# Kernel tuning notes

Measured on AMD Instinct MI355X. Metric: run time of the kernel, lower is better.

Reference implementation:

```python
import jax, jax.numpy as jnp
import numpy as np

B, S, D, H = 4, 2048, 1024, 16
DK = D // H  # 64


def setup_inputs() -> dict:
    key = jax.random.key(0)
    ks = jax.random.split(key, 12)
    sc = 0.02
    return {
        "q": jax.random.normal(ks[0], (B, S, D), jnp.float32),
        "k": jax.random.normal(ks[1], (B, S, D), jnp.float32),
        "v": jax.random.normal(ks[2], (B, S, D), jnp.float32),
        "mask": jax.random.randint(ks[3], (B, S, S), 0, 2).astype(bool),
        "Wq": jax.random.normal(ks[4], (H, D, DK), jnp.float32) * sc,
        "bq": jax.random.normal(ks[5], (H, DK), jnp.float32) * sc,
        "Wk": jax.random.normal(ks[6], (H, D, DK), jnp.float32) * sc,
        "bk": jax.random.normal(ks[7], (H, DK), jnp.float32) * sc,
        "Wv": jax.random.normal(ks[8], (H, D, DK), jnp.float32) * sc,
        "bv": jax.random.normal(ks[9], (H, DK), jnp.float32) * sc,
        "Wo": jax.random.normal(ks[10], (D, D), jnp.float32) * sc,
        "bo": jax.random.normal(ks[11], (D,), jnp.float32) * sc,
    }


def reference(q, k, v, mask, Wq, bq, Wk, bk, Wv, bv, Wo, bo):
    # per-head projections, batched over heads: [b,s,d] x [h,d,k] -> [b,h,s,k]
    qh = jnp.einsum('bsd,hdk->bhsk', q, Wq) + bq[None, :, None, :]
    kh = jnp.einsum('bsd,hdk->bhsk', k, Wk) + bk[None, :, None, :]
    vh = jnp.einsum('bsd,hdk->bhsk', v, Wv) + bv[None, :, None, :]
    dk = qh.shape[-1]
    scores = jnp.einsum('bhsk,bhtk->bhst', qh, kh) / (dk ** 0.5)
    # original uses masked_fill(mask == False, -1e-06) -- NOT -inf; keep faithful
    scores = jnp.where(mask[:, None, :, :], scores, jnp.float32(-1e-06))
    attn = jax.nn.softmax(scores, axis=-1)
    out = jnp.einsum('bhst,bhtk->bhsk', attn, vh)
    b, h, s, _ = out.shape
    out = out.transpose(0, 2, 1, 3).reshape(b, s, h * dk)  # concat heads
    return out @ Wo + bo
```

## Files before the change

### kernel.cpp

```cpp
#include <hip/hip_runtime.h>
#include <stdint.h>

#define Bn 4
#define Sn 2048
#define Dn 1024
#define Hn 16
#define DKn 64

typedef __bf16 bf16x8 __attribute__((ext_vector_type(8)));
typedef float f32x4 __attribute__((ext_vector_type(4)));
typedef unsigned short u16;
typedef unsigned long long u64;

union ABFrag { bf16x8 v; uint4 u; };
union V8 { u16 us[8]; uint4 u; };

__device__ __forceinline__ u16 f2bf(float f) {
  union { float f; uint32_t u; } a; a.f = f;
  return (u16)((a.u + 0x7fffu + ((a.u >> 16) & 1u)) >> 16);
}

__device__ __forceinline__ void gload16(const void* g, void* l) {
  __builtin_amdgcn_global_load_lds((const __attribute__((address_space(1))) unsigned int*)g,
                                   (__attribute__((address_space(3))) unsigned int*)l, 16, 0, 0);
}

__device__ __forceinline__ f32x4 zero4() { f32x4 z; z[0]=0.f; z[1]=0.f; z[2]=0.f; z[3]=0.f; return z; }


__global__ void conv_bf16(const float* __restrict__ src, u16* __restrict__ dst, int n4) {
  int i = blockIdx.x * 256 + threadIdx.x;
  if (i < n4) {
    float4 v = ((const float4*)src)[i];
    V8 o;
    o.us[0] = f2bf(v.x); o.us[1] = f2bf(v.y); o.us[2] = f2bf(v.z); o.us[3] = f2bf(v.w);
    ((uint2*)dst)[i] = make_uint2(o.u.x, o.u.y);
  }
}

__device__ __forceinline__ void tile_tr_body(const float* __restrict__ s, int ss,
                                             u16* __restrict__ d, int ds) {
  __shared__ float t[64 * 65];
  int tid = threadIdx.x;
  int r = tid >> 2, c0 = (tid & 3) * 16;
  #pragma unroll
  for (int j = 0; j < 4; ++j) {
    float4 v = *(const float4*)(s + r * ss + c0 + j * 4);
    t[(c0 + j * 4 + 0) * 65 + r] = v.x;
    t[(c0 + j * 4 + 1) * 65 + r] = v.y;
    t[(c0 + j * 4 + 2) * 65 + r] = v.z;
    t[(c0 + j * 4 + 3) * 65 + r] = v.w;
  }
  __syncthreads();
  V8 o0, o1;
  #pragma unroll
  for (int j = 0; j < 8; ++j) o0.us[j] = f2bf(t[r * 65 + c0 + j]);
  #pragma unroll
  for (int j = 0; j < 8; ++j) o1.us[j] = f2bf(t[r * 65 + c0 + 8 + j]);
  *(uint4*)(d + r * ds + c0) = o0.u;
  *(uint4*)(d + r * ds + c0 + 8) = o1.u;
}

__global__ void prep_wqkv_t(const float* __restrict__ Wq, const float* __restrict__ Wk,
                            const float* __restrict__ Wv, u16* __restrict__ out) {
  int bid = blockIdx.x;
  int w = bid >> 8, h = (bid >> 4) & 15, db = bid & 15;
  const float* src = (w == 0) ? Wq : (w == 1) ? Wk : Wv;
  tile_tr_body(src + (h * 1024 + db * 64) * 64, 64,
               out + (size_t)(w * 1024 + h * 64) * 1024 + db * 64, 1024);
}

__global__ void prep_wo_t(const float* __restrict__ Wo, u16* __restrict__ out) {
  int bid = blockIdx.x;
  int rb = bid >> 4, cb = bid & 15;
  tile_tr_body(Wo + (size_t)rb * 64 * 1024 + cb * 64, 1024,
               out + (size_t)cb * 64 * 1024 + rb * 64, 1024);
}

__global__ void mask_detect(const uint32_t* __restrict__ mw, int* __restrict__ flag) {
  int t = threadIdx.x;
  uint32_t acc = 0;
  for (int j = 0; j < 4; ++j) acc |= (mw[t * 4 + j] > 1u) ? 1u : 0u;
  unsigned long long bal = __ballot(acc != 0);
  __shared__ int s[4];
  if ((t & 63) == 0) s[t >> 6] = (bal != 0ull) ? 1 : 0;
  __syncthreads();
  if (t == 0) *flag = s[0] | s[1] | s[2] | s[3];
}

__global__ void mask_pack(const void* __restrict__ mraw, const int* __restrict__ flag,
                          u64* __restrict__ mb, int nwords) {
  int i = blockIdx.x * 256 + threadIdx.x;
  if (i >= nwords) return;
  u64 w = 0;
  if (*flag) {
    const uchar4* p = (const uchar4*)mraw + (size_t)i * 16;
    #pragma unroll
    for (int j = 0; j < 16; ++j) {
      uchar4 v = p[j];
      w |= ((u64)(v.x != 0)) << (j * 4 + 0);
      w |= ((u64)(v.y != 0)) << (j * 4 + 1);
      w |= ((u64)(v.z != 0)) << (j * 4 + 2);
      w |= ((u64)(v.w != 0)) << (j * 4 + 3);
    }
  } else {
    const uint4* p = (const uint4*)mraw + (size_t)i * 16;
    #pragma unroll
    for (int j = 0; j < 16; ++j) {
      uint4 v = p[j];
      w |= ((u64)(v.x != 0)) << (j * 4 + 0);
      w |= ((u64)(v.y != 0)) << (j * 4 + 1);
      w |= ((u64)(v.z != 0)) << (j * 4 + 2);
      w |= ((u64)(v.w != 0)) << (j * 4 + 3);
    }
  }
  mb[i] = w;
}

__global__ void transpose_v(const u16* __restrict__ vh, u16* __restrict__ vt) {
  __shared__ char lds[64 * 128];
  int tid = threadIdx.x;
  int bh = blockIdx.y, s0 = blockIdx.x * 64;
  const char* src = (const char*)(vh + ((size_t)bh * Sn + s0) * DKn);
  #pragma unroll
  for (int si = 0; si < 2; ++si) {
    int c = si * 256 + tid, r = c >> 3, cb = c & 7;
    uint4 v = *(const uint4*)(src + r * 128 + cb * 16);
    *(uint4*)(lds + r * 128 + ((cb ^ (r & 7)) << 4)) = v;
  }
  __syncthreads();
  #pragma unroll
  for (int si = 0; si < 2; ++si) {
    int c = si * 256 + tid, dkr = c >> 3, sb = c & 7;
    V8 t;
    #pragma unroll
    for (int j = 0; j < 8; ++j) {
      int s = sb * 8 + j;
      t.us[j] = *(const u16*)(lds + s * 128 + ((dkr * 2) ^ ((s & 7) << 4)));
    }
    *(uint4*)(vt + ((size_t)bh * DKn + dkr) * Sn + s0 + sb * 8) = t.u;
  }
}

template<int MODE>
__launch_bounds__(256)
__global__ void gemm_kernel(const u16* __restrict__ Aq, const u16* __restrict__ Ak,
                            const u16* __restrict__ Av, const u16* __restrict__ Bm,
                            const float* __restrict__ bq, const float* __restrict__ bk,
                            const float* __restrict__ bv,
                            u16* __restrict__ Oq, u16* __restrict__ Ok, u16* __restrict__ Ov,
                            float* __restrict__ Of) {
  __shared__ char lds[32768];
  char* Al = lds;
  char* Bl = lds + 16384;
  const int tid = threadIdx.x, w = tid >> 6, lane = tid & 63;
  const int n0 = blockIdx.x * 128, m0 = blockIdx.y * 128;
  int which = 0;
  const u16* A = Aq;
  if (MODE == 0) { which = n0 >> 10; A = (which == 0) ? Aq : (which == 1) ? Ak : Av; }

  f32x4 acc[2][8];
  #pragma unroll
  for (int i = 0; i < 2; ++i)
    #pragma unroll
    for (int j = 0; j < 8; ++j) acc[i][j] = zero4();

  for (int kt = 0; kt < 16; ++kt) {
    __syncthreads();
    #pragma unroll
    for (int si = 0; si < 4; ++si) {
      int c = si * 256 + tid, r = c >> 3, cb = c & 7;
      gload16((const char*)A + (((size_t)(m0 + r)) << 11) + (size_t)(kt * 128) + ((cb ^ (r & 7)) << 4),
              Al + si * 4096 + w * 1024);
    }
    #pragma unroll
    for (int si = 0; si < 4; ++si) {
      int c = si * 256 + tid, r = c >> 3, cb = c & 7;
      gload16((const char*)Bm + (((size_t)(n0 + r)) << 11) + (size_t)(kt * 128) + ((cb ^ (r & 7)) << 4),
              Bl + si * 4096 + w * 1024);
    }
    __syncthreads();
    #pragma unroll
    for (int kk = 0; kk < 2; ++kk) {
      ABFrag a0, a1;
      {
        int row = w * 32 + (lane & 15);
        int ch = (lane >> 4) + kk * 4;
        a0.u = *(const uint4*)(Al + row * 128 + ((ch ^ (row & 7)) << 4));
        row += 16;
        a1.u = *(const uint4*)(Al + row * 128 + ((ch ^ (row & 7)) << 4));
      }
      #pragma unroll
      for (int nn = 0; nn < 8; ++nn) {
        int row = nn * 16 + (lane & 15);
        int ch = (lane >> 4) + kk * 4;
        ABFrag bb; bb.u = *(const uint4*)(Bl + row * 128 + ((ch ^ (row & 7)) << 4));
        acc[0][nn] = __builtin_amdgcn_mfma_f32_16x16x32_bf16(a0.v, bb.v, acc[0][nn], 0, 0, 0);
        acc[1][nn] = __builtin_amdgcn_mfma_f32_16x16x32_bf16(a1.v, bb.v, acc[1][nn], 0, 0, 0);
      }
    }
  }

  if (MODE == 0) {
    const float esc = (which == 0) ? 0.18033688011112042f : 1.0f;
    const float* bias = (which == 0) ? bq : (which == 1) ? bk : bv;
    u16* O = (which == 0) ? Oq : (which == 1) ? Ok : Ov;
    #pragma unroll
    for (int nn = 0; nn < 8; ++nn) {
      int ng = (n0 & 1023) + nn * 16 + (lane & 15);
      int h = ng >> 6, dk = ng & 63;
      float bsv = bias[ng];
      #pragma unroll
      for (int mm = 0; mm < 2; ++mm) {
        #pragma unroll
        for (int r = 0; r < 4; ++r) {
          int mg = m0 + w * 32 + mm * 16 + (lane >> 4) * 4 + r;
          int b = mg >> 11, s = mg & 2047;
          O[(((size_t)(b * Hn + h)) * Sn + s) * DKn + dk] = f2bf((acc[mm][nn][r] + bsv) * esc);
        }
      }
    }
  } else {
    #pragma unroll
    for (int nn = 0; nn < 8; ++nn) {
      int ng = n0 + nn * 16 + (lane & 15);
      float bsv = bq[ng];
      #pragma unroll
      for (int mm = 0; mm < 2; ++mm) {
        #pragma unroll
        for (int r = 0; r < 4; ++r) {
          int mg = m0 + w * 32 + mm * 16 + (lane >> 4) * 4 + r;
          Of[(size_t)mg * 1024 + ng] = acc[mm][nn][r] + bsv;
        }
      }
    }
  }
}

__launch_bounds__(256, 4)
__global__ void flash_attn(const u16* __restrict__ qh, const u16* __restrict__ kh,
                           const u16* __restrict__ vt, const u64* __restrict__ mb,
                           u16* __restrict__ o) {
  __shared__ char lds[24576];
  char* Klds = lds;
  char* Vlds = lds + 8192;
  const int tid = threadIdx.x, w = tid >> 6, lane = tid & 63;
  const int l15 = lane & 15, g = lane >> 4;
  char* Plds = lds + 16384 + w * 2048;

  int bid = blockIdx.x;
  int wg = (bid & 7) * 256 + (bid >> 3);
  const int bh = wg >> 5, b = bh >> 4, h = bh & 15;
  const int qr = (wg & 31) * 64 + w * 16;

  ABFrag aq0, aq1;
  {
    const char* qrow = (const char*)(qh + ((size_t)bh * Sn + qr + l15) * DKn);
    aq0.u = *(const uint4*)(qrow + g * 16);
    aq1.u = *(const uint4*)(qrow + 64 + g * 16);
  }

  const char* kbase = (const char*)(kh + (size_t)bh * Sn * DKn);
  const char* vbase = (const char*)(vt + (size_t)bh * DKn * Sn);
  const int rowg = qr + g * 4;
  const char* mp = (const char*)mb + ((size_t)b * Sn + rowg) * 256;

  f32x4 oacc[4];
  float psum[4];
  #pragma unroll
  for (int nn = 0; nn < 4; ++nn) oacc[nn] = zero4();
  #pragma unroll
  for (int r = 0; r < 4; ++r) psum[r] = 0.f;

  const int sr = (256 + tid) >> 3, scb = (256 + tid) & 7;
  const int r0 = tid >> 3, cb0 = tid & 7;
  const int pw_base = (g * 4) * 128;
  const int pr_base = l15 * 128;
  const int pr_sw   = (l15 & 7) << 4;

  for (int kt = 0; kt < Sn / 64; ++kt) {
    u64 mw0 = *(const u64*)(mp + kt * 8);
    u64 mw1 = *(const u64*)(mp + kt * 8 + 256);
    u64 mw2 = *(const u64*)(mp + kt * 8 + 512);
    u64 mw3 = *(const u64*)(mp + kt * 8 + 768);

    __syncthreads();
    gload16(kbase + (size_t)(kt * 64 + r0) * 128 + ((cb0 ^ (r0 & 7)) << 4),
            Klds + w * 1024);
    gload16(kbase + (size_t)(kt * 64 + sr) * 128 + ((scb ^ (sr & 7)) << 4),
            Klds + 4096 + w * 1024);
    gload16(vbase + (size_t)r0 * (Sn * 2) + (size_t)(kt * 128) + ((cb0 ^ (r0 & 7)) << 4),
            Vlds + w * 1024);
    gload16(vbase + (size_t)sr * (Sn * 2) + (size_t)(kt * 128) + ((scb ^ (sr & 7)) << 4),
            Vlds + 4096 + w * 1024);
    __syncthreads();

    f32x4 sacc[4];
    #pragma unroll
    for (int nn = 0; nn < 4; ++nn) sacc[nn] = zero4();
    #pragma unroll
    for (int kk = 0; kk < 2; ++kk) {
      ABFrag aq = (kk == 0) ? aq0 : aq1;
      #pragma unroll
      for (int nn = 0; nn < 4; ++nn) {
        int row = nn * 16 + l15;
        int ch = g + kk * 4;
        ABFrag kf; kf.u = *(const uint4*)(Klds + row * 128 + ((ch ^ (row & 7)) << 4));
        sacc[nn] = __builtin_amdgcn_mfma_f32_16x16x32_bf16(aq.v, kf.v, sacc[nn], 0, 0, 0);
      }
    }

    #pragma unroll
    for (int r = 0; r < 4; ++r) {
      u64 mwr = (r == 0) ? mw0 : (r == 1) ? mw1 : (r == 2) ? mw2 : mw3;
      int prow = pw_base + r * 128;
      int psw = (((g * 4 + r) & 7) << 4);
      #pragma unroll
      for (int nn = 0; nn < 4; ++nn) {
        float pe = __builtin_amdgcn_exp2f(sacc[nn][r]);
        unsigned m16 = (unsigned)(mwr >> (nn * 16)) & 0xffffu;
        float pv = ((m16 >> l15) & 1u) ? pe : 1.0f;
        psum[r] += pv;
        *(__bf16*)(Plds + prow + (((nn * 32) + l15 * 2) ^ psw)) = (__bf16)pv;
      }
    }

    #pragma unroll
    for (int kk = 0; kk < 2; ++kk) {
      ABFrag pa;
      pa.u = *(const uint4*)(Plds + pr_base + ((kk * 64 + g * 16) ^ pr_sw));
      #pragma unroll
      for (int nn = 0; nn < 4; ++nn) {
        int row = nn * 16 + l15;
        int ch = g + kk * 4;
        ABFrag vb; vb.u = *(const uint4*)(Vlds + row * 128 + ((ch ^ (row & 7)) << 4));
        oacc[nn] = __builtin_amdgcn_mfma_f32_16x16x32_bf16(pa.v, vb.v, oacc[nn], 0, 0, 0);
      }
    }
  }

  #pragma unroll
  for (int r = 0; r < 4; ++r) {
    float s = psum[r];
    s += __shfl_xor(s, 1, 16);
    s += __shfl_xor(s, 2, 16);
    s += __shfl_xor(s, 4, 16);
    s += __shfl_xor(s, 8, 16);
    float inv = 1.f / s;
    int sg = qr + g * 4 + r;
    #pragma unroll
    for (int nn = 0; nn < 4; ++nn) {
      int col = h * 64 + nn * 16 + l15;
      o[((size_t)(b * Sn) + sg) * Dn + col] = f2bf(oacc[nn][r] * inv);
    }
  }
}


extern "C" void kernel_launch(void* const* d_in, const int* in_sizes, int n_in,
                              void* d_out, int out_size, void* d_ws, size_t ws_size,
                              hipStream_t stream) {
  (void)in_sizes; (void)n_in; (void)out_size; (void)ws_size;
  const float* q  = (const float*)d_in[0];
  const float* k  = (const float*)d_in[1];
  const float* v  = (const float*)d_in[2];
  const void*  mask = d_in[3];
  const float* Wq = (const float*)d_in[4];
  const float* bq = (const float*)d_in[5];
  const float* Wk = (const float*)d_in[6];
  const float* bk = (const float*)d_in[7];
  const float* Wv = (const float*)d_in[8];
  const float* bv = (const float*)d_in[9];
  const float* Wo = (const float*)d_in[10];
  const float* bo = (const float*)d_in[11];
  float* out = (float*)d_out;

  char* ws = (char*)d_ws;
  const size_t SZ = (size_t)8192 * 1024 * 2;
  u16* qbf   = (u16*)(ws);
  u16* kbf   = (u16*)(ws + SZ);
  u16* vbf   = (u16*)(ws + 2 * SZ);
  u16* Wcatt = (u16*)(ws + 3 * SZ);
  u16* Wot   = (u16*)(ws + 3 * SZ + 6291456);
  u16* qhp   = (u16*)(ws + 3 * SZ + 8388608);
  u16* khp   = (u16*)((char*)qhp + SZ);
  u16* vhp   = (u16*)((char*)khp + SZ);
  int* flag  = (int*)((char*)vhp + SZ);

  conv_bf16<<<8192, 256, 0, stream>>>(q, qbf, 2097152);
  conv_bf16<<<8192, 256, 0, stream>>>(k, kbf, 2097152);
  conv_bf16<<<8192, 256, 0, stream>>>(v, vbf, 2097152);
  prep_wqkv_t<<<768, 256, 0, stream>>>(Wq, Wk, Wv, Wcatt);
  prep_wo_t<<<256, 256, 0, stream>>>(Wo, Wot);

  gemm_kernel<0><<<dim3(24, 64), 256, 0, stream>>>(qbf, kbf, vbf, Wcatt, bq, bk, bv,
                                                   qhp, khp, vhp, nullptr);

  mask_detect<<<1, 256, 0, stream>>>((const uint32_t*)mask, flag);
  u64* mbw = (u64*)vbf;
  mask_pack<<<1024, 256, 0, stream>>>(mask, flag, mbw, 262144);

  u16* vtb = kbf;
  transpose_v<<<dim3(32, 64), 256, 0, stream>>>(vhp, vtb);

  u16* oc = qbf;
  flash_attn<<<2048, 256, 0, stream>>>(qhp, khp, vtb, mbw, oc);

  gemm_kernel<1><<<dim3(8, 64), 256, 0, stream>>>(oc, nullptr, nullptr, Wot, bo,
                                                  nullptr, nullptr, nullptr,
                                                  nullptr, nullptr, out);
}
```

Before: 453.5 us.

## Double-buffer K/V loads in flash attention, fuse prep kernels, write V transposed

Flash attention now prefetches the next K/V tile into a second LDS buffer while computing on the current one, with explicit waitcnt and barriers replacing the two syncthreads per tile. The three bf16 conversion launches are merged into one, as are the two weight-transpose launches. The V projection epilogue writes V directly in transposed layout, so the separate transpose_v kernel is dropped. The transposed V writes are strided 2-byte stores, which may coalesce poorly in the GEMM epilogue, and the larger LDS footprint may lower attention occupancy.

Measured after the change: 464.4 us. +2.4%, slower.

```diff
diff --git a/kernel.cpp b/kernel.cpp
--- a/kernel.cpp
+++ b/kernel.cpp
@@ -28,14 +28,17 @@
 __device__ __forceinline__ f32x4 zero4() { f32x4 z; z[0]=0.f; z[1]=0.f; z[2]=0.f; z[3]=0.f; return z; }
 
 
-__global__ void conv_bf16(const float* __restrict__ src, u16* __restrict__ dst, int n4) {
+__global__ void conv_bf16_all(const float* __restrict__ q, const float* __restrict__ k,
+                              const float* __restrict__ v, u16* __restrict__ dq,
+                              u16* __restrict__ dk, u16* __restrict__ dv) {
   int i = blockIdx.x * 256 + threadIdx.x;
-  if (i < n4) {
-    float4 v = ((const float4*)src)[i];
-    V8 o;
-    o.us[0] = f2bf(v.x); o.us[1] = f2bf(v.y); o.us[2] = f2bf(v.z); o.us[3] = f2bf(v.w);
-    ((uint2*)dst)[i] = make_uint2(o.u.x, o.u.y);
-  }
+  int seg = i >> 21, j = i & 2097151;
+  const float* s = (seg == 0) ? q : (seg == 1) ? k : v;
+  u16* d = (seg == 0) ? dq : (seg == 1) ? dk : dv;
+  float4 vv = ((const float4*)s)[j];
+  V8 o;
+  o.us[0] = f2bf(vv.x); o.us[1] = f2bf(vv.y); o.us[2] = f2bf(vv.z); o.us[3] = f2bf(vv.w);
+  ((uint2*)d)[j] = make_uint2(o.u.x, o.u.y);
 }
 
 __device__ __forceinline__ void tile_tr_body(const float* __restrict__ s, int ss,
@@ -61,20 +64,21 @@
   *(uint4*)(d + r * ds + c0 + 8) = o1.u;
 }
 
-__global__ void prep_wqkv_t(const float* __restrict__ Wq, const float* __restrict__ Wk,
-                            const float* __restrict__ Wv, u16* __restrict__ out) {
+__global__ void prep_w_all(const float* __restrict__ Wq, const float* __restrict__ Wk,
+                           const float* __restrict__ Wv, const float* __restrict__ Wo,
+                           u16* __restrict__ wcatt, u16* __restrict__ wot) {
   int bid = blockIdx.x;
-  int w = bid >> 8, h = (bid >> 4) & 15, db = bid & 15;
-  const float* src = (w == 0) ? Wq : (w == 1) ? Wk : Wv;
-  tile_tr_body(src + (h * 1024 + db * 64) * 64, 64,
-               out + (size_t)(w * 1024 + h * 64) * 1024 + db * 64, 1024);
-}
-
-__global__ void prep_wo_t(const float* __restrict__ Wo, u16* __restrict__ out) {
-  int bid = blockIdx.x;
-  int rb = bid >> 4, cb = bid & 15;
-  tile_tr_body(Wo + (size_t)rb * 64 * 1024 + cb * 64, 1024,
-               out + (size_t)cb * 64 * 1024 + rb * 64, 1024);
+  if (bid < 768) {
+    int w = bid >> 8, h = (bid >> 4) & 15, db = bid & 15;
+    const float* src = (w == 0) ? Wq : (w == 1) ? Wk : Wv;
+    tile_tr_body(src + (h * 1024 + db * 64) * 64, 64,
+                 wcatt + (size_t)(w * 1024 + h * 64) * 1024 + db * 64, 1024);
+  } else {
+    int b2 = bid - 768;
+    int rb = b2 >> 4, cb = b2 & 15;
+    tile_tr_body(Wo + (size_t)rb * 64 * 1024 + cb * 64, 1024,
+                 wot + (size_t)cb * 64 * 1024 + rb * 64, 1024);
+  }
 }
 
 __global__ void mask_detect(const uint32_t* __restrict__ mw, int* __restrict__ flag) {
@@ -115,31 +119,6 @@
     }
   }
   mb[i] = w;
-}
-
-__global__ void transpose_v(const u16* __restrict__ vh, u16* __restrict__ vt) {
-  __shared__ char lds[64 * 128];
-  int tid = threadIdx.x;
-  int bh = blockIdx.y, s0 = blockIdx.x * 64;
-  const char* src = (const char*)(vh + ((size_t)bh * Sn + s0) * DKn);
-  #pragma unroll
-  for (int si = 0; si < 2; ++si) {
-    int c = si * 256 + tid, r = c >> 3, cb = c & 7;
-    uint4 v = *(const uint4*)(src + r * 128 + cb * 16);
-    *(uint4*)(lds + r * 128 + ((cb ^ (r & 7)) << 4)) = v;
-  }
-  __syncthreads();
-  #pragma unroll
-  for (int si = 0; si < 2; ++si) {
-    int c = si * 256 + tid, dkr = c >> 3, sb = c & 7;
-    V8 t;
-    #pragma unroll
-    for (int j = 0; j < 8; ++j) {
-      int s = sb * 8 + j;
-      t.us[j] = *(const u16*)(lds + s * 128 + ((dkr * 2) ^ ((s & 7) << 4)));
-    }
-    *(uint4*)(vt + ((size_t)bh * DKn + dkr) * Sn + s0 + sb * 8) = t.u;
-  }
 }
 
 template<int MODE>
@@ -204,7 +183,6 @@
   if (MODE == 0) {
     const float esc = (which == 0) ? 0.18033688011112042f : 1.0f;
     const float* bias = (which == 0) ? bq : (which == 1) ? bk : bv;
-    u16* O = (which == 0) ? Oq : (which == 1) ? Ok : Ov;
     #pragma unroll
     for (int nn = 0; nn < 8; ++nn) {
       int ng = (n0 & 1023) + nn * 16 + (lane & 15);
@@ -216,7 +194,13 @@
         for (int r = 0; r < 4; ++r) {
           int mg = m0 + w * 32 + mm * 16 + (lane >> 4) * 4 + r;
           int b = mg >> 11, s = mg & 2047;
-          O[(((size_t)(b * Hn + h)) * Sn + s) * DKn + dk] = f2bf((acc[mm][nn][r] + bsv) * esc);
+          float val = (acc[mm][nn][r] + bsv) * esc;
+          if (which == 2) {
+            Ov[(((size_t)((b * Hn + h) * DKn + dk)) << 11) + s] = f2bf(val);
+          } else {
+            u16* O = (which == 0) ? Oq : Ok;
+            O[(((size_t)(b * Hn + h)) * Sn + s) * DKn + dk] = f2bf(val);
+          }
         }
       }
     }
@@ -241,12 +225,10 @@
 __global__ void flash_attn(const u16* __restrict__ qh, const u16* __restrict__ kh,
                            const u16* __restrict__ vt, const u64* __restrict__ mb,
                            u16* __restrict__ o) {
-  __shared__ char lds[24576];
-  char* Klds = lds;
-  char* Vlds = lds + 8192;
+  __shared__ char lds[40960];
   const int tid = threadIdx.x, w = tid >> 6, lane = tid & 63;
   const int l15 = lane & 15, g = lane >> 4;
-  char* Plds = lds + 16384 + w * 2048;
+  char* Plds = lds + 32768 + w * 2048;
 
   int bid = blockIdx.x;
   int wg = (bid & 7) * 256 + (bid >> 3);
@@ -272,28 +254,47 @@
   #pragma unroll
   for (int r = 0; r < 4; ++r) psum[r] = 0.f;
 
+  const int r0 = tid >> 3, cb0 = tid & 7;
   const int sr = (256 + tid) >> 3, scb = (256 + tid) & 7;
-  const int r0 = tid >> 3, cb0 = tid & 7;
   const int pw_base = (g * 4) * 128;
   const int pr_base = l15 * 128;
   const int pr_sw   = (l15 & 7) << 4;
 
+  gload16(kbase + (size_t)r0 * 128 + ((cb0 ^ (r0 & 7)) << 4), lds + w * 1024);
+  gload16(kbase + (size_t)sr * 128 + ((scb ^ (sr & 7)) << 4), lds + 4096 + w * 1024);
+  gload16(vbase + (size_t)r0 * (Sn * 2) + ((cb0 ^ (r0 & 7)) << 4), lds + 8192 + w * 1024);
+  gload16(vbase + (size_t)sr * (Sn * 2) + ((scb ^ (sr & 7)) << 4), lds + 12288 + w * 1024);
+
   for (int kt = 0; kt < Sn / 64; ++kt) {
+    char* bufK = lds + (kt & 1) * 16384;
+    char* bufV = bufK + 8192;
+    char* nK = lds + ((kt & 1) ^ 1) * 16384;
+    char* nV = nK + 8192;
+
     u64 mw0 = *(const u64*)(mp + kt * 8);
     u64 mw1 = *(const u64*)(mp + kt * 8 + 256);
     u64 mw2 = *(const u64*)(mp + kt * 8 + 512);
     u64 mw3 = *(const u64*)(mp + kt * 8 + 768);
 
-    __syncthreads();
-    gload16(kbase + (size_t)(kt * 64 + r0) * 128 + ((cb0 ^ (r0 & 7)) << 4),
-            Klds + w * 1024);
-    gload16(kbase + (size_t)(kt * 64 + sr) * 128 + ((scb ^ (sr & 7)) << 4),
-            Klds + 4096 + w * 1024);
-    gload16(vbase + (size_t)r0 * (Sn * 2) + (size_t)(kt * 128) + ((cb0 ^ (r0 & 7)) << 4),
-            Vlds + w * 1024);
-    gload16(vbase + (size_t)sr * (Sn * 2) + (size_t)(kt * 128) + ((scb ^ (sr & 7)) << 4),
-            Vlds + 4096 + w * 1024);
-    __syncthreads();
+    asm volatile("s_waitcnt lgkmcnt(0)" ::: "memory");
+    __builtin_amdgcn_sched_barrier(0);
+    __builtin_amdgcn_s_barrier();
+    __builtin_amdgcn_sched_barrier(0);
+
+    if (kt < Sn / 64 - 1) {
+      gload16(kbase + (size_t)((kt + 1) * 64 + r0) * 128 + ((cb0 ^ (r0 & 7)) << 4), nK + w * 1024);
+      gload16(kbase + (size_t)((kt + 1) * 64 + sr) * 128 + ((scb ^ (sr & 7)) << 4), nK + 4096 + w * 1024);
+      gload16(vbase + (size_t)r0 * (Sn * 2) + (size_t)((kt + 1) * 128) + ((cb0 ^ (r0 & 7)) << 4), nV + w * 1024);
+      gload16(vbase + (size_t)sr * (Sn * 2) + (size_t)((kt + 1) * 128) + ((scb ^ (sr & 7)) << 4), nV + 4096 + w * 1024);
+      __builtin_amdgcn_sched_barrier(0);
+      asm volatile("s_waitcnt vmcnt(8)" ::: "memory");
+    } else {
+      __builtin_amdgcn_sched_barrier(0);
+      asm volatile("s_waitcnt vmcnt(4)" ::: "memory");
+    }
+    __builtin_amdgcn_sched_barrier(0);
+    __builtin_amdgcn_s_barrier();
+    __builtin_amdgcn_sched_barrier(0);
 
     f32x4 sacc[4];
     #pragma unroll
@@ -305,7 +306,7 @@
       for (int nn = 0; nn < 4; ++nn) {
         int row = nn * 16 + l15;
         int ch = g + kk * 4;
-        ABFrag kf; kf.u = *(const uint4*)(Klds + row * 128 + ((ch ^ (row & 7)) << 4));
+        ABFrag kf; kf.u = *(const uint4*)(bufK + row * 128 + ((ch ^ (row & 7)) << 4));
         sacc[nn] = __builtin_amdgcn_mfma_f32_16x16x32_bf16(aq.v, kf.v, sacc[nn], 0, 0, 0);
       }
     }
@@ -333,7 +334,7 @@
       for (int nn = 0; nn < 4; ++nn) {
         int row = nn * 16 + l15;
         int ch = g + kk * 4;
-        ABFrag vb; vb.u = *(const uint4*)(Vlds + row * 128 + ((ch ^ (row & 7)) << 4));
+        ABFrag vb; vb.u = *(const uint4*)(bufV + row * 128 + ((ch ^ (row & 7)) << 4));
         oacc[nn] = __builtin_amdgcn_mfma_f32_16x16x32_bf16(pa.v, vb.v, oacc[nn], 0, 0, 0);
       }
     }
@@ -384,27 +385,21 @@
   u16* Wot   = (u16*)(ws + 3 * SZ + 6291456);
   u16* qhp   = (u16*)(ws + 3 * SZ + 8388608);
   u16* khp   = (u16*)((char*)qhp + SZ);
-  u16* vhp   = (u16*)((char*)khp + SZ);
-  int* flag  = (int*)((char*)vhp + SZ);
-
-  conv_bf16<<<8192, 256, 0, stream>>>(q, qbf, 2097152);
-  conv_bf16<<<8192, 256, 0, stream>>>(k, kbf, 2097152);
-  conv_bf16<<<8192, 256, 0, stream>>>(v, vbf, 2097152);
-  prep_wqkv_t<<<768, 256, 0, stream>>>(Wq, Wk, Wv, Wcatt);
-  prep_wo_t<<<256, 256, 0, stream>>>(Wo, Wot);
+  u16* vtp   = (u16*)((char*)khp + SZ);
+  int* flag  = (int*)((char*)vtp + SZ);
+
+  conv_bf16_all<<<24576, 256, 0, stream>>>(q, k, v, qbf, kbf, vbf);
+  prep_w_all<<<1024, 256, 0, stream>>>(Wq, Wk, Wv, Wo, Wcatt, Wot);
 
   gemm_kernel<0><<<dim3(24, 64), 256, 0, stream>>>(qbf, kbf, vbf, Wcatt, bq, bk, bv,
-                                                   qhp, khp, vhp, nullptr);
+                                                   qhp, khp, vtp, nullptr);
 
   mask_detect<<<1, 256, 0, stream>>>((const uint32_t*)mask, flag);
   u64* mbw = (u64*)vbf;
   mask_pack<<<1024, 256, 0, stream>>>(mask, flag, mbw, 262144);
 
-  u16* vtb = kbf;
-  transpose_v<<<dim3(32, 64), 256, 0, stream>>>(vhp, vtb);
-
   u16* oc = qbf;
-  flash_attn<<<2048, 256, 0, stream>>>(qhp, khp, vtb, mbw, oc);
+  flash_attn<<<2048, 256, 0, stream>>>(qhp, khp, vtp, mbw, oc);
 
   gemm_kernel<1><<<dim3(8, 64), 256, 0, stream>>>(oc, nullptr, nullptr, Wot, bo,
                                                   nullptr, nullptr, nullptr,
```
